# Kernel optimization log

Measured on AMD Instinct MI355X. Metric: run time of the kernel, lower is better.

## Reference

```python
import jax, jax.numpy as jnp
import numpy as np

B, L, D_MODEL, N_HEADS = 8, 256, 2048, 8
D_HEAD = D_MODEL // N_HEADS  # 256 == L, required by DeltaRuleOperator broadcasting
ALPHA0, BETA0 = 0.1, 0.9      # delta_rule_strength, 1 - strength
LN_EPS = 1e-5


def setup_inputs() -> dict:
    k = jax.random.key(0)
    ks = jax.random.split(k, 8)
    s = 0.02
    return {
        "query": jax.random.normal(ks[0], (B, L, D_MODEL), jnp.float32),
        "key": jax.random.normal(ks[1], (B, L, D_MODEL), jnp.float32),
        "value": jax.random.normal(ks[2], (B, L, D_MODEL), jnp.float32),
        "Wq": jax.random.normal(ks[3], (D_MODEL, D_MODEL), jnp.float32) * s,
        "Wk": jax.random.normal(ks[4], (D_MODEL, D_MODEL), jnp.float32) * s,
        "Wv": jax.random.normal(ks[5], (D_MODEL, D_MODEL), jnp.float32) * s,
        "Wo": jax.random.normal(ks[6], (D_MODEL, D_MODEL), jnp.float32) * s,
        "bo": jnp.zeros((D_MODEL,), jnp.float32),
        "ln_g": jnp.ones((D_MODEL,), jnp.float32),
        "ln_b": jnp.zeros((D_MODEL,), jnp.float32),
        "alpha": jnp.asarray(ALPHA0, jnp.float32),
        "beta": jnp.asarray(BETA0, jnp.float32),
    }


def reference(query, key, value, Wq, Wk, Wv, Wo, bo, ln_g, ln_b, alpha, beta):
    Bs, Ls, D = query.shape
    H, Dh = N_HEADS, D // N_HEADS

    def proj(x, W):  # torch Linear: x @ W.T, split heads -> [B,H,L,Dh]
        return (x @ W.T).reshape(Bs, Ls, H, Dh).transpose(0, 2, 1, 3)

    Q = proj(query, Wq)
    K = proj(key, Wk)
    V = proj(value, Wv)

    # DeltaRuleOperator, applied sequentially per head (buffer mutates across heads)
    kv = jnp.einsum('bhld,bhmd->bhlm', K, V)  # [B,H,L,L] with L == Dh
    kv_heads = jnp.moveaxis(kv, 1, 0)          # [H,B,L,L]

    def cs_step(cs, kv_h):
        # cumulative_state = beta*cs + alpha*detach(mean(kv)); head uses pre-update cs
        new = beta * cs + alpha * jax.lax.stop_gradient(kv_h.mean(axis=(0, 1)))
        return new, cs

    _, cs_seq = jax.lax.scan(cs_step, jnp.zeros((Dh,), query.dtype), kv_heads)  # [H,Dh]
    cs_b = cs_seq[None, :, None, :]                       # [1,H,1,Dh]
    q_mod = Q * (cs_b + alpha * (kv - cs_b))              # delta-rule modulated queries

    # elu feature map
    phi = lambda x: jax.nn.elu(x) + 1.0
    pq, pk = phi(q_mod), phi(K)

    def time_major(x):  # [B,H,L,Dh] -> [L, B*H, Dh]
        return x.reshape(Bs * H, Ls, Dh).transpose(1, 0, 2)

    pq_t, pk_t, v_t = time_major(pq), time_major(pk), time_major(V)

    def step(carry, xs):
        S, Z = carry                        # S:[N,Dh,Dh], Z:[N,Dh]
        q_i, k_i, v_i = xs                  # each [N,Dh]
        S = S + k_i[:, :, None] * v_i[:, None, :]
        Z = Z + k_i
        num = jnp.einsum('nf,nfd->nd', q_i, S)
        den = jnp.maximum(jnp.sum(q_i * Z, axis=-1), 1e-8)
        return (S, Z), num / den[:, None]

    N = Bs * H
    S0 = jnp.zeros((N, Dh, Dh), query.dtype)
    Z0 = jnp.zeros((N, Dh), query.dtype)
    _, outs = jax.lax.scan(step, (S0, Z0), (pq_t, pk_t, v_t))  # [L,N,Dh]

    attn = outs.transpose(1, 0, 2).reshape(Bs, H, Ls, Dh)
    attn = attn.transpose(0, 2, 1, 3).reshape(Bs, Ls, D)       # concat heads

    o = attn @ Wo.T + bo                  # out_proj (dropout is identity in eval)
    x = query + o                          # residual + LayerNorm
    mu = x.mean(-1, keepdims=True)
    var = jnp.mean((x - mu) ** 2, axis=-1, keepdims=True)
    return (x - mu) / jnp.sqrt(var + LN_EPS) * ln_g + ln_b
```

## Files before the change

### kernel.cpp

```cpp
#include <hip/hip_runtime.h>
#include <hip/hip_bf16.h>

using u16 = unsigned short;

typedef __bf16 bf16x8 __attribute__((ext_vector_type(8)));
typedef float  f32x4  __attribute__((ext_vector_type(4)));

__device__ __forceinline__ float b2f(u16 u) {
  union { unsigned u; float f; } v; v.u = ((unsigned)u) << 16; return v.f;
}
__device__ __forceinline__ u16 f2b(float f) {
  union { float f; unsigned u; } v; v.f = f;
  unsigned r = v.u + 0x7fffu + ((v.u >> 16) & 1u);
  return (u16)(r >> 16);
}

__device__ __forceinline__ void gld_lds16(const void* g, void* l) {
  __builtin_amdgcn_global_load_lds(
      (__attribute__((address_space(1))) void*)(unsigned long long)(g),
      (__attribute__((address_space(3))) void*)(unsigned long long)(l),
      16, 0, 0);
}

template <int EPI>
__global__ __launch_bounds__(256) void gemm_bt(
    const u16* __restrict__ A, int lda, long sA1, long sA2,
    const u16* __restrict__ B, int ldb, long sB1, long sB2,
    void* __restrict__ Cv, int ldc, long sC1, long sC2,
    int K, int HDIV,
    const float* __restrict__ bias, const float* __restrict__ resid) {
  __shared__ __align__(16) u16 lds[16384];
  __shared__ float denS[128];
  const int t = threadIdx.x;
  const int lane = t & 63;
  const int wave = t >> 6;
  const int wm = wave >> 1, wn = wave & 1;
  const int laneM = lane & 15, quad = lane >> 4;
  const int zb = blockIdx.z / HDIV, zh = blockIdx.z % HDIV;

  int bx = blockIdx.x, by = blockIdx.y;
  if (EPI == 2) { by = (bx >= 1) ? 1 : 0; bx = (bx == 2) ? 1 : 0; }
  const int kEnd = (EPI == 3) ? ((by + 1) * 128 < K ? (by + 1) * 128 : K) : K;

  const u16* Abase = A + zb * sA1 + zh * sA2 + (long)by * 128 * lda;
  const u16* Bbase = B + zb * sB1 + zh * sB2 + (long)bx * 128 * ldb;

  const int sRow = t >> 3;
  const int sc = ((t & 7) ^ (sRow & 7)) * 8;

  f32x4 acc[4][4];
#pragma unroll
  for (int i = 0; i < 4; ++i)
#pragma unroll
    for (int j = 0; j < 4; ++j) acc[i][j] = (f32x4){0.f, 0.f, 0.f, 0.f};
  float dsum[4] = {0.f, 0.f, 0.f, 0.f};

  const int fragA = (wm * 64 + laneM) * 64;
  const int fragB = 8192 + (wn * 64 + laneM) * 64;
  const int pbase = laneM & 7;

  for (int k0 = 0; k0 < kEnd; k0 += 64) {
#pragma unroll
    for (int p = 0; p < 4; ++p)
      gld_lds16(Abase + (long)(p * 32 + sRow) * lda + k0 + sc,
                &lds[p * 2048 + t * 8]);
#pragma unroll
    for (int p = 0; p < 4; ++p)
      gld_lds16(Bbase + (long)(p * 32 + sRow) * ldb + k0 + sc,
                &lds[8192 + p * 2048 + t * 8]);
    __syncthreads();
    bf16x8 af[2][4], bfv[2][4];
#pragma unroll
    for (int kk = 0; kk < 2; ++kk) {
      const int perm8 = ((kk * 4 + quad) ^ pbase) * 8;
#pragma unroll
      for (int i = 0; i < 4; ++i) {
        af[kk][i] = *(const bf16x8*)&lds[fragA + i * 1024 + perm8];
        bfv[kk][i] = *(const bf16x8*)&lds[fragB + i * 1024 + perm8];
      }
    }
    if (EPI == 3) {
#pragma unroll
      for (int kk = 0; kk < 2; ++kk)
#pragma unroll
        for (int i = 0; i < 4; ++i) {
          union { bf16x8 v; u16 s[8]; } u; u.v = af[kk][i];
          float ds = 0.f;
#pragma unroll
          for (int e = 0; e < 8; ++e) ds += b2f(u.s[e]);
          dsum[i] += ds;
        }
    }
#pragma unroll
    for (int kk = 0; kk < 2; ++kk)
#pragma unroll
      for (int i = 0; i < 4; ++i)
#pragma unroll
        for (int j = 0; j < 4; ++j)
          acc[i][j] = __builtin_amdgcn_mfma_f32_16x16x32_bf16(
              af[kk][i], bfv[kk][j], acc[i][j], 0, 0, 0);
    __syncthreads();
  }

  if (EPI == 3) {
#pragma unroll
    for (int i = 0; i < 4; ++i) {
      float s = dsum[i];
      s += __shfl_xor(s, 16);
      s += __shfl_xor(s, 32);
      if (wn == 0 && quad == 0)
        denS[wm * 64 + i * 16 + laneM] = fmaxf(s, 1e-8f);
    }
    __syncthreads();
  }

  const long cOff = zb * sC1 + zh * sC2;
  const int colB = bx * 128 + wn * 64;
#pragma unroll
  for (int i = 0; i < 4; ++i) {
#pragma unroll
    for (int j = 0; j < 4; ++j) {
#pragma unroll
      for (int r = 0; r < 4; ++r) {
        const int lrow = wm * 64 + i * 16 + quad * 4 + r;
        const int row = by * 128 + lrow;
        const int col = colB + j * 16 + laneM;
        const long idx = cOff + (long)row * ldc + col;
        float v = acc[i][j][r];
        if (EPI == 0) {
          ((u16*)Cv)[idx] = f2b(v);
        } else if (EPI == 1) {
          ((float*)Cv)[idx] = v;
        } else if (EPI == 2) {
          ((u16*)Cv)[idx] = f2b(col <= row ? v : 0.0f);
        } else if (EPI == 3) {
          ((u16*)Cv)[idx] = f2b(v / denS[lrow]);
        } else {
          ((float*)Cv)[idx] =
              (zb == 0) ? v + bias[col] + resid[(long)row * ldc + col] : v;
        }
      }
    }
  }
}

__global__ __launch_bounds__(256) void convert7(
    const float* __restrict__ s0, const float* __restrict__ s1,
    const float* __restrict__ s2, const float* __restrict__ s3,
    const float* __restrict__ s4, const float* __restrict__ s5,
    const float* __restrict__ s6, u16* __restrict__ dst) {
  long idx = (long)blockIdx.x * 256 + threadIdx.x;
  int seg = (int)(idx >> 20);
  long off = (idx & 1048575) << 2;
  const float* s;
  switch (seg) {
    case 0: s = s0; break; case 1: s = s1; break; case 2: s = s2; break;
    case 3: s = s3; break; case 4: s = s4; break; case 5: s = s5; break;
    default: s = s6;
  }
  float4 v = *(const float4*)(s + off);
  ushort4 o;
  o.x = f2b(v.x); o.y = f2b(v.y); o.z = f2b(v.z); o.w = f2b(v.w);
  *(ushort4*)(dst + (long)seg * 4194304 + off) = o;
}

__global__ __launch_bounds__(256) void kv_mean_partial(
    const float* __restrict__ kv, float* __restrict__ part) {
  int h = blockIdx.x, chunk = blockIdx.y, m = threadIdx.x;
  float acc = 0.f;
  for (int g = chunk * 128; g < chunk * 128 + 128; ++g) {
    int b = g >> 8, l = g & 255;
    acc += kv[(((long)(b * 8 + h) * 256) + l) * 256 + m];
  }
  part[(h * 16 + chunk) * 256 + m] = acc;
}

__global__ __launch_bounds__(256) void cs_kernel(
    const float* __restrict__ part, float* __restrict__ cs,
    const float* __restrict__ alphaP, const float* __restrict__ betaP) {
  int m = threadIdx.x;
  float alpha = *alphaP, beta = *betaP;
  float c = 0.f;
  for (int h = 0; h < 8; ++h) {
    cs[h * 256 + m] = c;
    float s = 0.f;
    for (int ch = 0; ch < 16; ++ch) s += part[(h * 16 + ch) * 256 + m];
    c = beta * c + alpha * (s * (1.0f / 2048.0f));
  }
}

__global__ __launch_bounds__(256) void pqpk_kernel(
    const u16* __restrict__ Qp, const u16* __restrict__ Kp,
    const float* __restrict__ kv, const float* __restrict__ cs,
    const float* __restrict__ alphaP, u16* __restrict__ pq,
    u16* __restrict__ pk) {
  long idx = (long)blockIdx.x * 256 + threadIdx.x;
  int d = idx & 255, l = (int)((idx >> 8) & 255), h = (int)((idx >> 16) & 7),
      b = (int)(idx >> 19);
  float alpha = *alphaP;
  long pidx = ((long)(b * 256 + l)) * 2048 + h * 256 + d;
  float Qv = b2f(Qp[pidx]);
  float kvv = kv[idx];
  float csv = cs[h * 256 + d];
  float qm = Qv * (csv + alpha * (kvv - csv));
  pq[idx] = f2b(qm > 0.f ? qm + 1.f : expf(qm));
  float Kv = b2f(Kp[pidx]);
  pk[idx] = f2b(Kv > 0.f ? Kv + 1.f : expf(Kv));
}

__global__ __launch_bounds__(256) void vtrans_kernel(const u16* __restrict__ Vp,
                                                     u16* __restrict__ Vt) {
  __shared__ u16 tile[32][33];
  int z = blockIdx.z, b = z >> 3, h = z & 7;
  int jT = blockIdx.x * 32, dT = blockIdx.y * 32;
  int tx = threadIdx.x, ty = threadIdx.y;
#pragma unroll
  for (int ii = 0; ii < 4; ++ii) {
    int j = jT + ty + ii * 8, d = dT + tx;
    tile[ty + ii * 8][tx] = Vp[(long)(b * 256 + j) * 2048 + h * 256 + d];
  }
  __syncthreads();
#pragma unroll
  for (int ii = 0; ii < 4; ++ii) {
    int d = dT + ty + ii * 8, j = jT + tx;
    Vt[(long)z * 65536 + d * 256 + j] = tile[tx][ty + ii * 8];
  }
}

__global__ __launch_bounds__(256) void ln_kernel(
    const float* __restrict__ x0, const float* __restrict__ x1,
    const float* __restrict__ g, const float* __restrict__ bb,
    float* __restrict__ out) {
  int row = blockIdx.x, t = threadIdx.x;
  const float4* xr0 = (const float4*)(x0 + (long)row * 2048);
  const float4* xr1 = (const float4*)(x1 + (long)row * 2048);
  float4 a0 = xr0[t], b0 = xr1[t], a1 = xr0[t + 256], b1 = xr1[t + 256];
  float4 v0, v1;
  v0.x = a0.x + b0.x; v0.y = a0.y + b0.y; v0.z = a0.z + b0.z; v0.w = a0.w + b0.w;
  v1.x = a1.x + b1.x; v1.y = a1.y + b1.y; v1.z = a1.z + b1.z; v1.w = a1.w + b1.w;
  float s = v0.x + v0.y + v0.z + v0.w + v1.x + v1.y + v1.z + v1.w;
  float ss = v0.x * v0.x + v0.y * v0.y + v0.z * v0.z + v0.w * v0.w +
             v1.x * v1.x + v1.y * v1.y + v1.z * v1.z + v1.w * v1.w;
  for (int o = 32; o; o >>= 1) { s += __shfl_xor(s, o); ss += __shfl_xor(ss, o); }
  __shared__ float a1s[4], a2s[4];
  int wave = t >> 6, lane = t & 63;
  if (lane == 0) { a1s[wave] = s; a2s[wave] = ss; }
  __syncthreads();
  s = a1s[0] + a1s[1] + a1s[2] + a1s[3];
  ss = a2s[0] + a2s[1] + a2s[2] + a2s[3];
  float mu = s * (1.f / 2048.f);
  float var = ss * (1.f / 2048.f) - mu * mu;
  float rstd = rsqrtf(var + 1e-5f);
  const float4* g4 = (const float4*)g;
  const float4* b4 = (const float4*)bb;
  float4* orow = (float4*)(out + (long)row * 2048);
  float4 gg = g4[t], bv = b4[t], r;
  r.x = (v0.x - mu) * rstd * gg.x + bv.x;
  r.y = (v0.y - mu) * rstd * gg.y + bv.y;
  r.z = (v0.z - mu) * rstd * gg.z + bv.z;
  r.w = (v0.w - mu) * rstd * gg.w + bv.w;
  orow[t] = r;
  gg = g4[t + 256]; bv = b4[t + 256];
  r.x = (v1.x - mu) * rstd * gg.x + bv.x;
  r.y = (v1.y - mu) * rstd * gg.y + bv.y;
  r.z = (v1.z - mu) * rstd * gg.z + bv.z;
  r.w = (v1.w - mu) * rstd * gg.w + bv.w;
  orow[t + 256] = r;
}

extern "C" void kernel_launch(void* const* d_in, const int* in_sizes, int n_in,
                              void* d_out, int out_size, void* d_ws,
                              size_t ws_size, hipStream_t stream) {
  const float* query = (const float*)d_in[0];
  const float* key = (const float*)d_in[1];
  const float* value = (const float*)d_in[2];
  const float* Wq = (const float*)d_in[3];
  const float* Wk = (const float*)d_in[4];
  const float* Wv = (const float*)d_in[5];
  const float* Wo = (const float*)d_in[6];
  const float* bo = (const float*)d_in[7];
  const float* ln_g = (const float*)d_in[8];
  const float* ln_b = (const float*)d_in[9];
  const float* alphaP = (const float*)d_in[10];
  const float* betaP = (const float*)d_in[11];

  char* ws = (char*)d_ws;
  const long SZ = 8388608;
  u16* qb = (u16*)(ws);
  u16* Wb = (u16*)(ws + 3 * SZ);
  u16* Qp = (u16*)(ws + 7 * SZ);
  float* kvf = (float*)(ws + 10 * SZ);
  u16* pq = (u16*)(ws + 12 * SZ);
  u16* pk = (u16*)(ws + 13 * SZ);
  u16* Vt = (u16*)(ws + 14 * SZ);
  u16* attnb = (u16*)(ws + 15 * SZ);
  u16* Ab = (u16*)(ws + 10 * SZ);
  float* x0 = (float*)(ws + 12 * SZ);
  float* x1 = (float*)(ws);
  float* part = (float*)(ws + 16 * SZ);
  float* cs = (float*)(ws + 16 * SZ + 16384);

  u16* Kp = Qp + 4194304;
  u16* Vp = Qp + 8388608;
  u16* Wob = Wb + 3 * 4194304;

  convert7<<<28672, 256, 0, stream>>>(query, key, value, Wq, Wk, Wv, Wo, qb);

  gemm_bt<0><<<dim3(16, 16, 3), 256, 0, stream>>>(
      qb, 2048, 4194304L, 0L, Wb, 2048, 4194304L, 0L, (void*)Qp, 2048,
      4194304L, 0L, 2048, 1, nullptr, nullptr);

  gemm_bt<1><<<dim3(2, 2, 64), 256, 0, stream>>>(
      Kp, 2048, 524288L, 256L, Vp, 2048, 524288L, 256L, (void*)kvf, 256,
      524288L, 65536L, 256, 8, nullptr, nullptr);

  kv_mean_partial<<<dim3(8, 16), 256, 0, stream>>>(kvf, part);
  cs_kernel<<<1, 256, 0, stream>>>(part, cs, alphaP, betaP);

  pqpk_kernel<<<16384, 256, 0, stream>>>(Qp, Kp, kvf, cs, alphaP, pq, pk);

  gemm_bt<2><<<dim3(3, 1, 64), 256, 0, stream>>>(
      pq, 256, 524288L, 65536L, pk, 256, 524288L, 65536L, (void*)Ab, 256,
      524288L, 65536L, 256, 8, nullptr, nullptr);

  vtrans_kernel<<<dim3(8, 8, 64), dim3(32, 8), 0, stream>>>(Vp, Vt);

  gemm_bt<3><<<dim3(2, 2, 64), 256, 0, stream>>>(
      Ab, 256, 524288L, 65536L, Vt, 256, 524288L, 65536L, (void*)attnb, 2048,
      524288L, 256L, 256, 8, nullptr, nullptr);

  gemm_bt<4><<<dim3(16, 16, 2), 256, 0, stream>>>(
      attnb, 2048, 1024L, 0L, Wob, 2048, 1024L, 0L, (void*)x0, 2048,
      -25165824L, 0L, 1024, 1, bo, query);

  ln_kernel<<<2048, 256, 0, stream>>>(x0, x1, ln_g, ln_b, (float*)d_out);
}
```

Before: 345.7 us.

## Fuse kv column-mean into KV GEMM epilogue, store kv as bf16, use BK=32 for big GEMMs

Adds a BK template parameter to the GEMM and selects a 32-wide K tile for the two large projection GEMMs, which halves LDS use and may raise occupancy. The KV GEMM epilogue now reduces its accumulators per column and atomically adds them into a per-head partial sum, so the separate kv_mean_partial pass over the fp32 kv buffer is gone. kv is stored as bf16 instead of fp32, which halves that write and the later read in pqpk. In exchange there is a memset, float atomics that make the summation order nondeterministic, and bf16 rounding of kv before the delta-rule modulation.

```diff
diff --git a/kernel.cpp b/kernel.cpp
--- a/kernel.cpp
+++ b/kernel.cpp
@@ -22,14 +22,15 @@
       16, 0, 0);
 }
 
-template <int EPI>
+template <int EPI, int BK>
 __global__ __launch_bounds__(256) void gemm_bt(
     const u16* __restrict__ A, int lda, long sA1, long sA2,
     const u16* __restrict__ B, int ldb, long sB1, long sB2,
     void* __restrict__ Cv, int ldc, long sC1, long sC2,
     int K, int HDIV,
-    const float* __restrict__ bias, const float* __restrict__ resid) {
-  __shared__ __align__(16) u16 lds[16384];
+    const float* __restrict__ bias, const float* __restrict__ resid,
+    float* __restrict__ partOut) {
+  __shared__ __align__(16) u16 lds[2 * 128 * BK];
   __shared__ float denS[128];
   const int t = threadIdx.x;
   const int lane = t & 63;
@@ -45,8 +46,13 @@
   const u16* Abase = A + zb * sA1 + zh * sA2 + (long)by * 128 * lda;
   const u16* Bbase = B + zb * sB1 + zh * sB2 + (long)bx * 128 * ldb;
 
-  const int sRow = t >> 3;
-  const int sc = ((t & 7) ^ (sRow & 7)) * 8;
+  constexpr int STEPS = BK / 16;
+  constexpr int RPS = 2048 / BK;
+  constexpr int KK = BK / 32;
+  const int sRow = (BK == 64) ? (t >> 3) : (t >> 2);
+  const int sg = (BK == 64) ? (t & 7) : (t & 3);
+  const int swz = (BK == 64) ? (sg ^ (sRow & 7)) : (sg ^ ((sRow >> 1) & 3));
+  const int sc = swz * 8;
 
   f32x4 acc[4][4];
 #pragma unroll
@@ -55,33 +61,32 @@
     for (int j = 0; j < 4; ++j) acc[i][j] = (f32x4){0.f, 0.f, 0.f, 0.f};
   float dsum[4] = {0.f, 0.f, 0.f, 0.f};
 
-  const int fragA = (wm * 64 + laneM) * 64;
-  const int fragB = 8192 + (wn * 64 + laneM) * 64;
-  const int pbase = laneM & 7;
-
-  for (int k0 = 0; k0 < kEnd; k0 += 64) {
-#pragma unroll
-    for (int p = 0; p < 4; ++p)
-      gld_lds16(Abase + (long)(p * 32 + sRow) * lda + k0 + sc,
+  for (int k0 = 0; k0 < kEnd; k0 += BK) {
+#pragma unroll
+    for (int p = 0; p < STEPS; ++p)
+      gld_lds16(Abase + (long)(p * RPS + sRow) * lda + k0 + sc,
                 &lds[p * 2048 + t * 8]);
 #pragma unroll
-    for (int p = 0; p < 4; ++p)
-      gld_lds16(Bbase + (long)(p * 32 + sRow) * ldb + k0 + sc,
-                &lds[8192 + p * 2048 + t * 8]);
+    for (int p = 0; p < STEPS; ++p)
+      gld_lds16(Bbase + (long)(p * RPS + sRow) * ldb + k0 + sc,
+                &lds[128 * BK + p * 2048 + t * 8]);
     __syncthreads();
-    bf16x8 af[2][4], bfv[2][4];
-#pragma unroll
-    for (int kk = 0; kk < 2; ++kk) {
-      const int perm8 = ((kk * 4 + quad) ^ pbase) * 8;
+    bf16x8 af[KK][4], bfv[KK][4];
+#pragma unroll
+    for (int kk = 0; kk < KK; ++kk) {
+      int perm8;
+      if (BK == 64) perm8 = ((kk * 4 + quad) ^ (laneM & 7)) * 8;
+      else          perm8 = (quad ^ ((laneM >> 1) & 3)) * 8;
 #pragma unroll
       for (int i = 0; i < 4; ++i) {
-        af[kk][i] = *(const bf16x8*)&lds[fragA + i * 1024 + perm8];
-        bfv[kk][i] = *(const bf16x8*)&lds[fragB + i * 1024 + perm8];
+        af[kk][i] = *(const bf16x8*)&lds[(wm * 64 + i * 16 + laneM) * BK + perm8];
+        bfv[kk][i] =
+            *(const bf16x8*)&lds[128 * BK + (wn * 64 + i * 16 + laneM) * BK + perm8];
       }
     }
     if (EPI == 3) {
 #pragma unroll
-      for (int kk = 0; kk < 2; ++kk)
+      for (int kk = 0; kk < KK; ++kk)
 #pragma unroll
         for (int i = 0; i < 4; ++i) {
           union { bf16x8 v; u16 s[8]; } u; u.v = af[kk][i];
@@ -92,7 +97,7 @@
         }
     }
 #pragma unroll
-    for (int kk = 0; kk < 2; ++kk)
+    for (int kk = 0; kk < KK; ++kk)
 #pragma unroll
       for (int i = 0; i < 4; ++i)
 #pragma unroll
@@ -114,6 +119,21 @@
     __syncthreads();
   }
 
+  if (EPI == 1) {
+#pragma unroll
+    for (int j = 0; j < 4; ++j) {
+      float s = 0.f;
+#pragma unroll
+      for (int i = 0; i < 4; ++i)
+#pragma unroll
+        for (int r = 0; r < 4; ++r) s += acc[i][j][r];
+      s += __shfl_xor(s, 16);
+      s += __shfl_xor(s, 32);
+      if (quad == 0)
+        atomicAdd(&partOut[zh * 256 + bx * 128 + wn * 64 + j * 16 + laneM], s);
+    }
+  }
+
   const long cOff = zb * sC1 + zh * sC2;
   const int colB = bx * 128 + wn * 64;
 #pragma unroll
@@ -127,10 +147,8 @@
         const int col = colB + j * 16 + laneM;
         const long idx = cOff + (long)row * ldc + col;
         float v = acc[i][j][r];
-        if (EPI == 0) {
+        if (EPI == 0 || EPI == 1) {
           ((u16*)Cv)[idx] = f2b(v);
-        } else if (EPI == 1) {
-          ((float*)Cv)[idx] = v;
         } else if (EPI == 2) {
           ((u16*)Cv)[idx] = f2b(col <= row ? v : 0.0f);
         } else if (EPI == 3) {
@@ -164,17 +182,6 @@
   *(ushort4*)(dst + (long)seg * 4194304 + off) = o;
 }
 
-__global__ __launch_bounds__(256) void kv_mean_partial(
-    const float* __restrict__ kv, float* __restrict__ part) {
-  int h = blockIdx.x, chunk = blockIdx.y, m = threadIdx.x;
-  float acc = 0.f;
-  for (int g = chunk * 128; g < chunk * 128 + 128; ++g) {
-    int b = g >> 8, l = g & 255;
-    acc += kv[(((long)(b * 8 + h) * 256) + l) * 256 + m];
-  }
-  part[(h * 16 + chunk) * 256 + m] = acc;
-}
-
 __global__ __launch_bounds__(256) void cs_kernel(
     const float* __restrict__ part, float* __restrict__ cs,
     const float* __restrict__ alphaP, const float* __restrict__ betaP) {
@@ -183,15 +190,13 @@
   float c = 0.f;
   for (int h = 0; h < 8; ++h) {
     cs[h * 256 + m] = c;
-    float s = 0.f;
-    for (int ch = 0; ch < 16; ++ch) s += part[(h * 16 + ch) * 256 + m];
-    c = beta * c + alpha * (s * (1.0f / 2048.0f));
+    c = beta * c + alpha * (part[h * 256 + m] * (1.0f / 2048.0f));
   }
 }
 
 __global__ __launch_bounds__(256) void pqpk_kernel(
     const u16* __restrict__ Qp, const u16* __restrict__ Kp,
-    const float* __restrict__ kv, const float* __restrict__ cs,
+    const u16* __restrict__ kv, const float* __restrict__ cs,
     const float* __restrict__ alphaP, u16* __restrict__ pq,
     u16* __restrict__ pk) {
   long idx = (long)blockIdx.x * 256 + threadIdx.x;
@@ -200,7 +205,7 @@
   float alpha = *alphaP;
   long pidx = ((long)(b * 256 + l)) * 2048 + h * 256 + d;
   float Qv = b2f(Qp[pidx]);
-  float kvv = kv[idx];
+  float kvv = b2f(kv[idx]);
   float csv = cs[h * 256 + d];
   float qm = Qv * (csv + alpha * (kvv - csv));
   pq[idx] = f2b(qm > 0.f ? qm + 1.f : expf(qm));
@@ -289,7 +294,7 @@
   u16* qb = (u16*)(ws);
   u16* Wb = (u16*)(ws + 3 * SZ);
   u16* Qp = (u16*)(ws + 7 * SZ);
-  float* kvf = (float*)(ws + 10 * SZ);
+  u16* kvb = (u16*)(ws + 10 * SZ);
   u16* pq = (u16*)(ws + 12 * SZ);
   u16* pk = (u16*)(ws + 13 * SZ);
   u16* Vt = (u16*)(ws + 14 * SZ);
@@ -304,34 +309,35 @@
   u16* Vp = Qp + 8388608;
   u16* Wob = Wb + 3 * 4194304;
 
+  hipMemsetAsync(part, 0, 8 * 256 * sizeof(float), stream);
+
   convert7<<<28672, 256, 0, stream>>>(query, key, value, Wq, Wk, Wv, Wo, qb);
 
-  gemm_bt<0><<<dim3(16, 16, 3), 256, 0, stream>>>(
+  gemm_bt<0, 32><<<dim3(16, 16, 3), 256, 0, stream>>>(
       qb, 2048, 4194304L, 0L, Wb, 2048, 4194304L, 0L, (void*)Qp, 2048,
-      4194304L, 0L, 2048, 1, nullptr, nullptr);
-
-  gemm_bt<1><<<dim3(2, 2, 64), 256, 0, stream>>>(
-      Kp, 2048, 524288L, 256L, Vp, 2048, 524288L, 256L, (void*)kvf, 256,
-      524288L, 65536L, 256, 8, nullptr, nullptr);
-
-  kv_mean_partial<<<dim3(8, 16), 256, 0, stream>>>(kvf, part);
+      4194304L, 0L, 2048, 1, nullptr, nullptr, nullptr);
+
+  gemm_bt<1, 64><<<dim3(2, 2, 64), 256, 0, stream>>>(
+      Kp, 2048, 524288L, 256L, Vp, 2048, 524288L, 256L, (void*)kvb, 256,
+      524288L, 65536L, 256, 8, nullptr, nullptr, part);
+
   cs_kernel<<<1, 256, 0, stream>>>(part, cs, alphaP, betaP);
 
-  pqpk_kernel<<<16384, 256, 0, stream>>>(Qp, Kp, kvf, cs, alphaP, pq, pk);
-
-  gemm_bt<2><<<dim3(3, 1, 64), 256, 0, stream>>>(
+  pqpk_kernel<<<16384, 256, 0, stream>>>(Qp, Kp, kvb, cs, alphaP, pq, pk);
+
+  gemm_bt<2, 64><<<dim3(3, 1, 64), 256, 0, stream>>>(
       pq, 256, 524288L, 65536L, pk, 256, 524288L, 65536L, (void*)Ab, 256,
-      524288L, 65536L, 256, 8, nullptr, nullptr);
+      524288L, 65536L, 256, 8, nullptr, nullptr, nullptr);
 
   vtrans_kernel<<<dim3(8, 8, 64), dim3(32, 8), 0, stream>>>(Vp, Vt);
 
-  gemm_bt<3><<<dim3(2, 2, 64), 256, 0, stream>>>(
+  gemm_bt<3, 64><<<dim3(2, 2, 64), 256, 0, stream>>>(
       Ab, 256, 524288L, 65536L, Vt, 256, 524288L, 65536L, (void*)attnb, 2048,
-      524288L, 256L, 256, 8, nullptr, nullptr);
-
-  gemm_bt<4><<<dim3(16, 16, 2), 256, 0, stream>>>(
+      524288L, 256L, 256, 8, nullptr, nullptr, nullptr);
+
+  gemm_bt<4, 32><<<dim3(16, 16, 2), 256, 0, stream>>>(
       attnb, 2048, 1024L, 0L, Wob, 2048, 1024L, 0L, (void*)x0, 2048,
-      -25165824L, 0L, 1024, 1, bo, query);
+      -25165824L, 0L, 1024, 1, bo, query, nullptr);
 
   ln_kernel<<<2048, 256, 0, stream>>>(x0, x1, ln_g, ln_b, (float*)d_out);
 }
```

Result: faster. 332.0 us (-4.0%).
